# Kernel tuning notes

Measured on AMD Instinct MI355X. Metric: run time of the kernel, lower is better.

## Reference

```python
import jax, jax.numpy as jnp
import numpy as np

D = 1024
H = 16
HD = D // H
FF = 4096
EPS = 1e-5
B, L = 8, 1024

def setup_inputs() -> dict:
    key = jax.random.key(0)
    ks = jax.random.split(key, 12)
    s = lambda k, shape: jax.random.normal(k, shape, dtype=jnp.float32) * (shape[0] ** -0.5)
    return {
        "x": jax.random.normal(ks[0], (B, L, D), dtype=jnp.float32),
        "attention_mask": jnp.ones((B, L), dtype=jnp.int32),
        "wq": s(ks[1], (D, D)), "bq": jnp.zeros((D,), jnp.float32),
        "wk": s(ks[2], (D, D)), "bk": jnp.zeros((D,), jnp.float32),
        "wv": s(ks[3], (D, D)), "bv": jnp.zeros((D,), jnp.float32),
        "wo": s(ks[4], (D, D)), "bo": jnp.zeros((D,), jnp.float32),
        "ln1_s": jnp.ones((D,), jnp.float32), "ln1_b": jnp.zeros((D,), jnp.float32),
        "ln2_s": jnp.ones((D,), jnp.float32), "ln2_b": jnp.zeros((D,), jnp.float32),
        "w1": s(ks[5], (D, FF)), "b1": jnp.zeros((FF,), jnp.float32),
        "w2": s(ks[6], (FF, D)), "b2": jnp.zeros((D,), jnp.float32),
    }

def _layer_norm(x, scale, bias):
    mu = jnp.mean(x, axis=-1, keepdims=True)
    var = jnp.mean(jnp.square(x - mu), axis=-1, keepdims=True)
    return (x - mu) * jax.lax.rsqrt(var + EPS) * scale + bias

def _quick_gelu(x):
    return x * jax.nn.sigmoid(1.702 * x)

def reference(x, attention_mask, wq, bq, wk, bk, wv, bv, wo, bo,
              ln1_s, ln1_b, ln2_s, ln2_b, w1, b1, w2, b2):
    Bc, Lc, Dc = x.shape
    scale = HD ** -0.5
    # --- attention block (pre-LN) ---
    h = _layer_norm(x, ln1_s, ln1_b)
    to_heads = lambda t: t.reshape(Bc, Lc, H, HD).transpose(0, 2, 1, 3)
    q = to_heads(h @ wq + bq)
    k = to_heads(h @ wk + bk)
    v = to_heads(h @ wv + bv)
    scores = jnp.einsum('bhqd,bhkd->bhqk', q.astype(jnp.float32), k.astype(jnp.float32)) * scale
    fmask = jnp.where(attention_mask[:, None, None, :] > 0, 0.0,
                      jnp.finfo(scores.dtype).min)
    weights = jax.nn.softmax(scores + fmask, axis=-1)
    attn = jnp.einsum('bhqk,bhkd->bhqd', weights, v.astype(jnp.float32))
    attn = attn.transpose(0, 2, 1, 3).reshape(Bc, Lc, Dc).astype(x.dtype)
    x = x + (attn @ wo + bo)
    # --- MLP block (pre-LN) ---
    h = _layer_norm(x, ln2_s, ln2_b)
    h = _quick_gelu(h @ w1 + b1) @ w2 + b2
    return x + h
```

## Files before the change

kernel.cpp:

```cpp
#include <hip/hip_runtime.h>
#include <math.h>

#define D_MODEL 1024
#define N_TOK   8192
#define SEQ_L   1024
#define N_HEAD  16
#define HEAD_D  64
#define FF_DIM  4096

typedef __attribute__((ext_vector_type(8))) short bf16x8;
typedef __attribute__((ext_vector_type(4))) short short4v;
typedef __attribute__((ext_vector_type(2))) int  int2v;
typedef __attribute__((ext_vector_type(4))) float f32x4;

#define MFMA16(a, b, c) __builtin_amdgcn_mfma_f32_16x16x32_bf16((a), (b), (c), 0, 0, 0)

#define GLD16(gp, lp) __builtin_amdgcn_global_load_lds(                      \
    (const __attribute__((address_space(1))) void*)(gp),                     \
    (__attribute__((address_space(3))) void*)(lp), 16, 0, 0)

#if defined(__has_builtin)
#if __has_builtin(__builtin_amdgcn_exp2f)
#define EXP2F(x) __builtin_amdgcn_exp2f(x)
#else
#define EXP2F(x) exp2f(x)
#endif
#else
#define EXP2F(x) exp2f(x)
#endif

__device__ __forceinline__ short f2bf(float f) {
    unsigned u = __float_as_uint(f);
    u += 0x7fffu + ((u >> 16) & 1u);
    return (short)(u >> 16);
}

__device__ __forceinline__ int pack2bf(float a, float b) {
    unsigned ua = __float_as_uint(a) + 0x8000u;
    unsigned ub = __float_as_uint(b) + 0x8000u;
    return __builtin_amdgcn_perm(ub, ua, 0x07060302u);
}

__global__ __launch_bounds__(256) void ln_kernel(const float* __restrict__ x,
                                                 const float* __restrict__ g,
                                                 const float* __restrict__ b,
                                                 short* __restrict__ o)
{
    int t = blockIdx.x;
    const float* xr = x + (size_t)t * D_MODEL;
    short* orow = o + (size_t)t * D_MODEL;
    float vals[4];
    float lsum = 0.f, lsq = 0.f;
#pragma unroll
    for (int i = 0; i < 4; i++) {
        float v = xr[threadIdx.x + i * 256];
        vals[i] = v; lsum += v; lsq += v * v;
    }
#pragma unroll
    for (int off = 32; off > 0; off >>= 1) {
        lsum += __shfl_down(lsum, off);
        lsq  += __shfl_down(lsq,  off);
    }
    __shared__ float red[8];
    int wid = threadIdx.x >> 6, lane = threadIdx.x & 63;
    if (lane == 0) { red[wid] = lsum; red[4 + wid] = lsq; }
    __syncthreads();
    if (threadIdx.x == 0) {
        red[0] = red[0] + red[1] + red[2] + red[3];
        red[4] = red[4] + red[5] + red[6] + red[7];
    }
    __syncthreads();
    float mean = red[0] * (1.f / D_MODEL);
    float var  = red[4] * (1.f / D_MODEL) - mean * mean;
    float inv  = rsqrtf(var + 1e-5f);
#pragma unroll
    for (int i = 0; i < 4; i++) {
        int c = threadIdx.x + i * 256;
        orow[c] = f2bf((vals[i] - mean) * inv * g[c] + b[c]);
    }
}

__global__ __launch_bounds__(256) void prep_kernel(
    const float* __restrict__ wq, const float* __restrict__ wk,
    const float* __restrict__ wv, const float* __restrict__ wo,
    const float* __restrict__ w1, const float* __restrict__ w2,
    const int*   __restrict__ amask,
    short* __restrict__ wqkvt, short* __restrict__ wot,
    short* __restrict__ w1t,  short* __restrict__ w2t,
    float* __restrict__ fmask)
{
    int id = blockIdx.x;
    if (id >= 12288) {
        int i = (id - 12288) * 256 + threadIdx.x;
        fmask[i] = (amask[i] > 0) ? 0.f : -1e30f;
        return;
    }
    const float* src; short* dst; int R, C, tloc, csh;
    if (id < 4096) {
        int wsel = id >> 10; tloc = id & 1023; R = 1024; C = 1024; csh = 5;
        src = (wsel == 0) ? wq : (wsel == 1) ? wk : (wsel == 2) ? wv : wo;
        dst = (wsel == 3) ? wot : (wqkvt + (size_t)wsel * 1024 * 1024);
    } else if (id < 8192) {
        tloc = id - 4096; R = 1024; C = 4096; csh = 7; src = w1; dst = w1t;
    } else {
        tloc = id - 8192; R = 4096; C = 1024; csh = 5; src = w2; dst = w2t;
    }
    int ty = tloc >> csh, tx = tloc & ((1 << csh) - 1);
    int r0 = ty * 32, c0 = tx * 32;
    __shared__ float t[32][33];
    int tid = threadIdx.x;
#pragma unroll
    for (int i = 0; i < 4; i++) {
        int idx = i * 256 + tid;
        int r = idx >> 5, c = idx & 31;
        t[r][c] = src[(size_t)(r0 + r) * C + c0 + c];
    }
    __syncthreads();
#pragma unroll
    for (int i = 0; i < 4; i++) {
        int idx = i * 256 + tid;
        int rr = idx >> 5, cc = idx & 31;
        dst[(size_t)(c0 + rr) * R + r0 + cc] = f2bf(t[cc][rr]);
    }
}

template<int DBUF>
__global__ __launch_bounds__(256) void gemm_bf16(
    const short* __restrict__ A, int lda,
    const short* __restrict__ Bt, int ldb,
    const float* __restrict__ bias,
    const float* __restrict__ bias2,
    const float* __restrict__ bias3,
    const float* __restrict__ resid,
    float* __restrict__ Cf, short* __restrict__ Cb, short* __restrict__ Cvt,
    int ldc, int K, int act, int qkv, int gx)
{
    __shared__ __align__(16) short sA[(1 + DBUF) * 8192];
    __shared__ __align__(16) short sB[(1 + DBUF) * 8192];
    const int tid = threadIdx.x;
    const int lane = tid & 63, wave = tid >> 6;
    const int quad = lane >> 4, l15 = lane & 15;

    const int id = blockIdx.x;
    const int xcd = id & 7, j = id >> 3;
    const int bx = j % gx, by = xcd + 8 * (j / gx);
    const int bm = by * 128, bn = bx * 128;
    const int wm = (wave >> 1) * 64, wn = (wave & 1) * 64;

    const int lr = lane >> 3;
    const int lc = (lane & 7) ^ lr;
    const int sw = l15 & 7;

    const short* Ab = A  + (size_t)(bm + wave * 32 + lr) * lda + lc * 8;
    const short* Bb = Bt + (size_t)(bn + wave * 32 + lr) * ldb + lc * 8;

    f32x4 acc[4][4];
#pragma unroll
    for (int i = 0; i < 4; i++)
#pragma unroll
        for (int jj = 0; jj < 4; jj++) acc[i][jj] = (f32x4){0.f, 0.f, 0.f, 0.f};

    const int nk = K >> 6;

    if (DBUF) {
#pragma unroll
        for (int c = 0; c < 4; c++) {
            int cid = wave * 4 + c;
            GLD16(Ab + (size_t)(c * 8) * lda, &sA[cid * 512]);
            GLD16(Bb + (size_t)(c * 8) * ldb, &sB[cid * 512]);
        }
    }

    for (int ki = 0; ki < nk; ki++) {
        __syncthreads();
        if (DBUF) {
            if (ki + 1 < nk) {
                int k0 = (ki + 1) << 6, nb = (ki + 1) & 1;
#pragma unroll
                for (int c = 0; c < 4; c++) {
                    int cid = wave * 4 + c;
                    GLD16(Ab + (size_t)(c * 8) * lda + k0, &sA[nb * 8192 + cid * 512]);
                    GLD16(Bb + (size_t)(c * 8) * ldb + k0, &sB[nb * 8192 + cid * 512]);
                }
            }
        } else {
            int k0 = ki << 6;
#pragma unroll
            for (int c = 0; c < 4; c++) {
                int cid = wave * 4 + c;
                GLD16(Ab + (size_t)(c * 8) * lda + k0, &sA[cid * 512]);
                GLD16(Bb + (size_t)(c * 8) * ldb + k0, &sB[cid * 512]);
            }
            __syncthreads();
        }
        const short* cA = &sA[DBUF ? (ki & 1) * 8192 : 0];
        const short* cB = &sB[DBUF ? (ki & 1) * 8192 : 0];
#pragma unroll
        for (int ko = 0; ko < 2; ko++) {
            bf16x8 af[4], bfr[4];
#pragma unroll
            for (int mt = 0; mt < 4; mt++) {
                int row = wm + mt * 16 + l15;
                af[mt] = *(const bf16x8*)&cA[(row * 8 + ((ko * 4 + quad) ^ sw)) * 8];
            }
#pragma unroll
            for (int nt = 0; nt < 4; nt++) {
                int row = wn + nt * 16 + l15;
                bfr[nt] = *(const bf16x8*)&cB[(row * 8 + ((ko * 4 + quad) ^ sw)) * 8];
            }
#pragma unroll
            for (int mt = 0; mt < 4; mt++)
#pragma unroll
                for (int nt = 0; nt < 4; nt++)
                    acc[mt][nt] = MFMA16(af[mt], bfr[nt], acc[mt][nt]);
        }
    }

#pragma unroll
    for (int mt = 0; mt < 4; mt++)
#pragma unroll
        for (int nt = 0; nt < 4; nt++) {
            int row0 = bm + wm + mt * 16 + quad * 4;
            int col  = bn + wn + nt * 16 + l15;
            if (qkv) {
                int seg = col >> 10, cloc = col & 1023;
                const float* bp = (seg == 0) ? bias : (seg == 1) ? bias2 : bias3;
                float bval = bp[cloc];
                if (seg == 2) {
                    int bb = row0 >> 10, l0 = row0 & 1023;
                    size_t page = (size_t)(bb * N_HEAD + (cloc >> 6)) * HEAD_D + (cloc & 63);
                    short4v pk = { f2bf(acc[mt][nt][0] + bval), f2bf(acc[mt][nt][1] + bval),
                                   f2bf(acc[mt][nt][2] + bval), f2bf(acc[mt][nt][3] + bval) };
                    *(short4v*)&Cvt[page * SEQ_L + l0] = pk;
                } else {
                    short* dst = Cb + (size_t)seg * ((size_t)N_TOK * D_MODEL);
#pragma unroll
                    for (int r = 0; r < 4; r++)
                        dst[(size_t)(row0 + r) * D_MODEL + cloc] = f2bf(acc[mt][nt][r] + bval);
                }
            } else {
#pragma unroll
                for (int r = 0; r < 4; r++) {
                    int row = row0 + r;
                    float v = acc[mt][nt][r] + bias[col];
                    if (act) v = v / (1.f + __expf(-1.702f * v));
                    if (resid) v += resid[(size_t)row * ldc + col];
                    if (Cb) Cb[(size_t)row * ldc + col] = f2bf(v);
                    else    Cf[(size_t)row * ldc + col] = v;
                }
            }
        }
}

__global__ __launch_bounds__(256) void attn_kernel(
    const short* __restrict__ Q, const short* __restrict__ Kb,
    const short* __restrict__ Vt, const float* __restrict__ fmask,
    short* __restrict__ O)
{
    __shared__ __align__(16) short sK[8192];
    __shared__ __align__(16) short sV[8192];
    __shared__ __align__(16) short sP[4][32 * 136];
    __shared__ __align__(16) float sAl[4][2][20];

    const int g = blockIdx.x;
    const int xcd = g & 7, slot = g >> 3;
    const int qt = slot & 7, bhl = slot >> 3;
    const int bh = xcd * 16 + bhl;
    const int b = bh >> 4, h = bh & 15;

    const int tid = threadIdx.x;
    const int wave = tid >> 6, lane = tid & 63;
    const int quad = lane >> 4, l15 = lane & 15;

    const int qbase = b * SEQ_L + qt * 128;
    bf16x8 qf[2][2];
#pragma unroll
    for (int qh = 0; qh < 2; qh++) {
        const short* qp = Q + (size_t)(qbase + wave * 32 + qh * 16 + l15) * D_MODEL
                        + h * HEAD_D + quad * 8;
        qf[qh][0] = *(const bf16x8*)qp;
        qf[qh][1] = *(const bf16x8*)(qp + 32);
    }

    const short* Kbh = Kb + (size_t)b * SEQ_L * D_MODEL + h * HEAD_D;
    const short* Vbh = Vt + (size_t)(b * N_HEAD + h) * HEAD_D * SEQ_L;
    const float* mk  = fmask + b * SEQ_L;

    f32x4 o4[2][4];
#pragma unroll
    for (int qh = 0; qh < 2; qh++)
#pragma unroll
        for (int nt = 0; nt < 4; nt++) o4[qh][nt] = (f32x4){0.f, 0.f, 0.f, 0.f};
    float mrow[2] = {-1e30f, -1e30f}, lrow[2] = {0.f, 0.f};
    short* pslab = &sP[wave][0];
    const float CSC = 0.125f * 1.4426950408889634f;

    for (int kt = 0; kt < SEQ_L / 128; kt++) {
        __syncthreads();
#pragma unroll
        for (int j = 0; j < 4; j++) {
            int cid = wave * 4 + j;
            int kc = cid >> 1, key0 = (cid & 1) << 6;
            GLD16(Kbh + (size_t)(kt * 128 + key0 + lane) * D_MODEL + kc * 8,
                  &sK[cid * 512]);
            GLD16(Vbh + (size_t)lane * SEQ_L + kt * 128 + cid * 8,
                  &sV[cid * 512]);
        }
        __syncthreads();

        f32x4 mkv[8];
#pragma unroll
        for (int sub = 0; sub < 8; sub++)
            mkv[sub] = *(const f32x4*)&mk[kt * 128 + sub * 16 + quad * 4];

        f32x4 s[8][2];
#pragma unroll
        for (int sub = 0; sub < 8; sub++) {
            bf16x8 kf0 = *(const bf16x8*)&sK[(quad * 128 + sub * 16 + l15) * 8];
            bf16x8 kf1 = *(const bf16x8*)&sK[((quad + 4) * 128 + sub * 16 + l15) * 8];
#pragma unroll
            for (int qh = 0; qh < 2; qh++) {
                s[sub][qh] = (f32x4){0.f, 0.f, 0.f, 0.f};
                s[sub][qh] = MFMA16(kf0, qf[qh][0], s[sub][qh]);
                s[sub][qh] = MFMA16(kf1, qf[qh][1], s[sub][qh]);
            }
        }
        float alpha[2];
#pragma unroll
        for (int qh = 0; qh < 2; qh++) {
#pragma unroll
            for (int sub = 0; sub < 8; sub++)
#pragma unroll
                for (int r = 0; r < 4; r++)
                    s[sub][qh][r] = s[sub][qh][r] * CSC + mkv[sub][r];
            f32x4 mx4 = s[0][qh];
#pragma unroll
            for (int sub = 1; sub < 8; sub++)
#pragma unroll
                for (int r = 0; r < 4; r++) mx4[r] = fmaxf(mx4[r], s[sub][qh][r]);
            float pmax = fmaxf(fmaxf(mx4[0], mx4[1]), fmaxf(mx4[2], mx4[3]));
            pmax = fmaxf(pmax, __shfl_xor(pmax, 16));
            pmax = fmaxf(pmax, __shfl_xor(pmax, 32));
            float mnew = fmaxf(mrow[qh], pmax);
            alpha[qh] = EXP2F(mrow[qh] - mnew);
            mrow[qh] = mnew;
            if (quad == 0) sAl[wave][qh][l15] = alpha[qh];

            float ls = 0.f;
#pragma unroll
            for (int sub = 0; sub < 8; sub++) {
                float p0 = EXP2F(s[sub][qh][0] - mnew);
                float p1 = EXP2F(s[sub][qh][1] - mnew);
                float p2 = EXP2F(s[sub][qh][2] - mnew);
                float p3 = EXP2F(s[sub][qh][3] - mnew);
                ls += (p0 + p1) + (p2 + p3);
                int2v pk = { pack2bf(p0, p1), pack2bf(p2, p3) };
                *(int2v*)&pslab[(qh * 16 + l15) * 136 + sub * 16 + quad * 4] = pk;
            }
            ls += __shfl_xor(ls, 16);
            ls += __shfl_xor(ls, 32);
            lrow[qh] = lrow[qh] * alpha[qh] + ls;
        }

#pragma unroll
        for (int qh = 0; qh < 2; qh++) {
            f32x4 av = *(const f32x4*)&sAl[wave][qh][quad * 4];
#pragma unroll
            for (int nt = 0; nt < 4; nt++)
#pragma unroll
                for (int r = 0; r < 4; r++) o4[qh][nt][r] *= av[r];
        }

        bf16x8 pf[2][4];
#pragma unroll
        for (int qh = 0; qh < 2; qh++)
#pragma unroll
            for (int c = 0; c < 4; c++)
                pf[qh][c] = *(const bf16x8*)&pslab[(qh * 16 + l15) * 136 + c * 32 + quad * 8];
#pragma unroll
        for (int nt = 0; nt < 4; nt++)
#pragma unroll
            for (int c = 0; c < 4; c++) {
                bf16x8 vfr = *(const bf16x8*)&sV[((c * 4 + quad) * 64 + nt * 16 + l15) * 8];
                o4[0][nt] = MFMA16(pf[0][c], vfr, o4[0][nt]);
                o4[1][nt] = MFMA16(pf[1][c], vfr, o4[1][nt]);
            }
    }
    if (quad == 0) {
        sAl[wave][0][l15] = 1.f / lrow[0];
        sAl[wave][1][l15] = 1.f / lrow[1];
    }
    __syncthreads();
#pragma unroll
    for (int qh = 0; qh < 2; qh++) {
        f32x4 iv = *(const f32x4*)&sAl[wave][qh][quad * 4];
#pragma unroll
        for (int nt = 0; nt < 4; nt++)
#pragma unroll
            for (int r = 0; r < 4; r++)
                O[(size_t)(qbase + wave * 32 + qh * 16 + quad * 4 + r) * D_MODEL
                  + h * HEAD_D + nt * 16 + l15] = f2bf(o4[qh][nt][r] * iv[r]);
    }
}

extern "C" void kernel_launch(void* const* d_in, const int* in_sizes, int n_in,
                              void* d_out, int out_size, void* d_ws, size_t ws_size,
                              hipStream_t stream)
{
    const float* x     = (const float*)d_in[0];
    const int*   amask = (const int*)  d_in[1];
    const float* wq    = (const float*)d_in[2];
    const float* bq    = (const float*)d_in[3];
    const float* wk    = (const float*)d_in[4];
    const float* bk    = (const float*)d_in[5];
    const float* wv    = (const float*)d_in[6];
    const float* bv    = (const float*)d_in[7];
    const float* wo    = (const float*)d_in[8];
    const float* bo    = (const float*)d_in[9];
    const float* ln1s  = (const float*)d_in[10];
    const float* ln1b  = (const float*)d_in[11];
    const float* ln2s  = (const float*)d_in[12];
    const float* ln2b  = (const float*)d_in[13];
    const float* w1    = (const float*)d_in[14];
    const float* b1    = (const float*)d_in[15];
    const float* w2    = (const float*)d_in[16];
    const float* b2    = (const float*)d_in[17];
    float* out = (float*)d_out;

    char* w = (char*)d_ws;
    short* wqkvt = (short*)(w + (size_t)0);
    short* wot   = (short*)(w + ((size_t)6  << 20));
    short* w1t   = (short*)(w + ((size_t)8  << 20));
    short* w2t   = (short*)(w + ((size_t)16 << 20));
    short* hb    = (short*)(w + ((size_t)24 << 20));
    short* qb    = (short*)(w + ((size_t)40 << 20));
    short* kbf   = (short*)(w + ((size_t)56 << 20));
    short* attnb = (short*)(w + ((size_t)72 << 20));
    short* vtb   = (short*)(w + ((size_t)88 << 20));
    short* ffb   = qb;
    float* fmaskb = (float*)d_out;

    dim3 blk(256);

    prep_kernel<<<dim3(12320), blk, 0, stream>>>(wq, wk, wv, wo, w1, w2, amask,
                                                 wqkvt, wot, w1t, w2t, fmaskb);

    ln_kernel<<<N_TOK, blk, 0, stream>>>(x, ln1s, ln1b, hb);

    gemm_bf16<0><<<dim3(24 * 64), blk, 0, stream>>>(
        hb, 1024, wqkvt, 1024, bq, bk, bv, nullptr,
        nullptr, qb, vtb, 1024, 1024, 0, 1, 24);

    attn_kernel<<<dim3(1024), blk, 0, stream>>>(qb, kbf, vtb, fmaskb, attnb);

    gemm_bf16<1><<<dim3(8 * 64), blk, 0, stream>>>(
        attnb, 1024, wot, 1024, bo, nullptr, nullptr, x,
        out, nullptr, nullptr, 1024, 1024, 0, 0, 8);

    ln_kernel<<<N_TOK, blk, 0, stream>>>(out, ln2s, ln2b, hb);

    gemm_bf16<0><<<dim3(32 * 64), blk, 0, stream>>>(
        hb, 1024, w1t, 1024, b1, nullptr, nullptr, nullptr,
        nullptr, ffb, nullptr, 4096, 1024, 1, 0, 32);
    gemm_bf16<1><<<dim3(8 * 64), blk, 0, stream>>>(
        ffb, 4096, w2t, 4096, b2, nullptr, nullptr, out,
        out, nullptr, nullptr, 1024, 4096, 0, 0, 8);
}
```

Baseline: 537.5 us.

## Add 256-row, 512-thread bf16 GEMM with phased double-buffered pipeline

Adds a new gemm256 kernel with 256xBN tiles, 8 waves, and a hand-scheduled ping-pong schedule. It interleaves LDS fragment reads, MFMA phases (with raised priority), and global-to-LDS async loads under explicit barriers and waitcnts. The QKV, FFN-up and FFN-down GEMMs now use it in place of the 128-tile gemm_bf16. Larger tiles raise arithmetic intensity and the overlap hides load latency, at the cost of fewer blocks, heavier register and LDS use, and many barriers. The epilogue copied into the old kernel contains an odd duplicated Cf store that looks like an editing slip.

Result: slower. 748.2 us (+39.2%).

```diff
diff --git a/kernel.cpp b/kernel.cpp
--- a/kernel.cpp
+++ b/kernel.cpp
@@ -220,6 +220,193 @@
     for (int mt = 0; mt < 4; mt++)
 #pragma unroll
         for (int nt = 0; nt < 4; nt++) {
+            int row0 = bm + wm + mt * 16 + quad * 4;
+            int col  = bn + wn + nt * 16 + l15;
+            if (qkv) {
+                int seg = col >> 10, cloc = col & 1023;
+                const float* bp = (seg == 0) ? bias : (seg == 1) ? bias2 : bias3;
+                float bval = bp[cloc];
+                if (seg == 2) {
+                    int bb = row0 >> 10, l0 = row0 & 1023;
+                    size_t page = (size_t)(bb * N_HEAD + (cloc >> 6)) * HEAD_D + (cloc & 63);
+                    short4v pk = { f2bf(acc[mt][nt][0] + bval), f2bf(acc[mt][nt][1] + bval),
+                                   f2bf(acc[mt][nt][2] + bval), f2bf(acc[mt][nt][3] + bval) };
+                    *(short4v*)&Cvt[page * SEQ_L + l0] = pk;
+                } else {
+                    short* dst = Cb + (size_t)seg * ((size_t)N_TOK * D_MODEL);
+#pragma unroll
+                    for (int r = 0; r < 4; r++)
+                        dst[(size_t)(row0 + r) * D_MODEL + cloc] = f2bf(acc[mt][nt][r] + bval);
+                }
+            } else {
+#pragma unroll
+                for (int r = 0; r < 4; r++) {
+                    int row = row0 + r;
+                    float v = acc[mt][nt][r] + bias[col];
+                    if (act) v = v / (1.f + __expf(-1.702f * v));
+                    if (resid) v += resid[(size_t)row * ldc + col];
+                    if (Cb) Cb[(size_t)row * ldc + col] = f2bf(v);
+                    else    Cf[(size_t)row * ldc + col] = f2bf(v), Cf[(size_t)row * ldc + col] = v;
+                }
+            }
+        }
+}
+
+#define BAR() __builtin_amdgcn_s_barrier()
+#define WAIT_LGKM0() do { asm volatile("s_waitcnt lgkmcnt(0)");               \
+                          __builtin_amdgcn_sched_barrier(0); } while (0)
+
+#define STA(buf, h, tt) do {                                                  \
+    const short* s_ = Asrc + (size_t)((h) * 128) * lda + (size_t)(tt) * 64;   \
+    GLD16(s_,                    &sAs[(buf)*16384 + (h)*8192        + wave*512]); \
+    GLD16(s_ + (size_t)64 * lda, &sAs[(buf)*16384 + (h)*8192 + 4096 + wave*512]); \
+} while (0)
+
+#define STB(buf, h, tt) do {                                                  \
+    if constexpr (NREP == 4) {                                                \
+        const short* s_ = Bsrc + (size_t)((h) * 128) * ldb + (size_t)(tt) * 64; \
+        GLD16(s_,                    &sBs[(buf)*16384 + (h)*8192        + wave*512]); \
+        GLD16(s_ + (size_t)64 * ldb, &sBs[(buf)*16384 + (h)*8192 + 4096 + wave*512]); \
+    } else {                                                                  \
+        const short* s_ = Bsrc + (size_t)((h) * 64) * ldb + (size_t)(tt) * 64; \
+        GLD16(s_, &sBs[(buf)*8192 + (h)*4096 + wave*512]);                    \
+    }                                                                         \
+} while (0)
+
+#define VMCNT() do {                                                          \
+    if constexpr (NREP == 4) asm volatile("s_waitcnt vmcnt(6)");              \
+    else                     asm volatile("s_waitcnt vmcnt(4)");              \
+} while (0)
+
+#define LDA_F(buf, mt, ko) (*(const bf16x8*)&sAs[(buf)*16384 +                \
+    (((wm + (mt)*16 + l15) << 3) + (((ko)*4 + quad) ^ sw)) * 8])
+#define LDB_F(buf, nt, ko) (*(const bf16x8*)&sBs[(buf)*(NREP == 4 ? 16384 : 8192) + \
+    (((wn + (nt)*16 + l15) << 3) + (((ko)*4 + quad) ^ sw)) * 8])
+
+#define PH_READ_B(buf)                                                        \
+    _Pragma("unroll")                                                         \
+    for (int nt = 0; nt < NREP; nt++) {                                       \
+        bfr[nt][0] = LDB_F(buf, nt, 0);                                       \
+        bfr[nt][1] = LDB_F(buf, nt, 1);                                       \
+    }
+#define PH_READ_A(buf, mh)                                                    \
+    _Pragma("unroll")                                                         \
+    for (int mt = 0; mt < 4; mt++) {                                          \
+        afr[mt][0] = LDA_F(buf, (mh)*4 + mt, 0);                              \
+        afr[mt][1] = LDA_F(buf, (mh)*4 + mt, 1);                              \
+    }
+#define PH_MFMA(mh, nh)                                                       \
+    __builtin_amdgcn_s_setprio(1);                                            \
+    _Pragma("unroll")                                                         \
+    for (int mt = 0; mt < 4; mt++)                                            \
+        _Pragma("unroll")                                                     \
+        for (int nt = 0; nt < NREP / 2; nt++) {                               \
+            acc[(mh)*4 + mt][(nh)*(NREP/2) + nt] =                            \
+                MFMA16(afr[mt][0], bfr[(nh)*(NREP/2) + nt][0],                \
+                       acc[(mh)*4 + mt][(nh)*(NREP/2) + nt]);                 \
+            acc[(mh)*4 + mt][(nh)*(NREP/2) + nt] =                            \
+                MFMA16(afr[mt][1], bfr[(nh)*(NREP/2) + nt][1],                \
+                       acc[(mh)*4 + mt][(nh)*(NREP/2) + nt]);                 \
+        }                                                                     \
+    __builtin_amdgcn_s_setprio(0);
+
+template<int NREP>
+__global__ __launch_bounds__(512, 2) void gemm256(
+    const short* __restrict__ A, int lda,
+    const short* __restrict__ Bt, int ldb,
+    const float* __restrict__ bias,
+    const float* __restrict__ bias2,
+    const float* __restrict__ bias3,
+    const float* __restrict__ resid,
+    float* __restrict__ Cf, short* __restrict__ Cb, short* __restrict__ Cvt,
+    int ldc, int K, int act, int qkv, int gx)
+{
+    constexpr int BN = NREP * 64;
+    __shared__ __align__(16) short sAs[2 * 256 * 64];
+    __shared__ __align__(16) short sBs[2 * BN  * 64];
+
+    const int tid  = threadIdx.x;
+    const int wave = tid >> 6, lane = tid & 63;
+    const int quad = lane >> 4, l15 = lane & 15;
+    const int wm = (wave >> 2) * 128;
+    const int wn = (wave & 3) * (NREP * 16);
+    const int sw = l15 & 7;
+
+    const int id = blockIdx.x;
+    const int xcd = id & 7, j = id >> 3;
+    const int bx = j % gx, by = xcd + 8 * (j / gx);
+    const int bm = by * 256, bn = bx * BN;
+
+    const int r_in = tid >> 3;
+    const int csrc = (tid & 7) ^ (r_in & 7);
+    const short* Asrc = A  + (size_t)(bm + r_in) * lda + csrc * 8;
+    const short* Bsrc = Bt + (size_t)(bn + r_in) * ldb + csrc * 8;
+
+    f32x4 acc[8][NREP];
+#pragma unroll
+    for (int i = 0; i < 8; i++)
+#pragma unroll
+        for (int jj = 0; jj < NREP; jj++) acc[i][jj] = (f32x4){0.f, 0.f, 0.f, 0.f};
+
+    const int nk = K >> 6;
+
+    STB(0, 0, 0); STB(0, 1, 0);
+    STA(0, 0, 0); STA(0, 1, 0);
+    STB(1, 0, 1); STB(1, 1, 1);
+    STA(1, 0, 1);
+    VMCNT();
+    BAR();
+
+    bf16x8 afr[4][2], bfr[NREP][2];
+
+    for (int it = 0; it < nk; it += 2) {
+        int t2 = it + 2; if (t2 >= nk) t2 -= nk;
+        int t3 = it + 3; if (t3 >= nk) t3 -= nk;
+
+        PH_READ_B(0); PH_READ_A(0, 0);
+        STA(1, 1, it + 1);
+        BAR(); WAIT_LGKM0();
+        PH_MFMA(0, 0);
+        BAR();
+        STB(0, 0, t2);
+        BAR();
+        PH_MFMA(0, 1);
+        BAR();
+        PH_READ_A(0, 1);
+        STB(0, 1, t2);
+        BAR(); WAIT_LGKM0();
+        PH_MFMA(1, 1);
+        BAR();
+        STA(0, 0, t2);
+        BAR();
+        PH_MFMA(1, 0);
+        VMCNT();
+        BAR();
+        PH_READ_B(1); PH_READ_A(1, 0);
+        STA(0, 1, t2);
+        BAR(); WAIT_LGKM0();
+        PH_MFMA(0, 0);
+        BAR();
+        STB(1, 0, t3);
+        BAR();
+        PH_MFMA(0, 1);
+        BAR();
+        PH_READ_A(1, 1);
+        STB(1, 1, t3);
+        BAR(); WAIT_LGKM0();
+        PH_MFMA(1, 1);
+        BAR();
+        STA(1, 0, t3);
+        BAR();
+        PH_MFMA(1, 0);
+        VMCNT();
+        BAR();
+    }
+
+#pragma unroll
+    for (int mt = 0; mt < 8; mt++)
+#pragma unroll
+        for (int nt = 0; nt < NREP; nt++) {
             int row0 = bm + wm + mt * 16 + quad * 4;
             int col  = bn + wn + nt * 16 + l15;
             if (qkv) {
@@ -440,16 +627,16 @@
     short* ffb   = qb;
     float* fmaskb = (float*)d_out;
 
-    dim3 blk(256);
+    dim3 blk(256), blk512(512);
 
     prep_kernel<<<dim3(12320), blk, 0, stream>>>(wq, wk, wv, wo, w1, w2, amask,
                                                  wqkvt, wot, w1t, w2t, fmaskb);
 
     ln_kernel<<<N_TOK, blk, 0, stream>>>(x, ln1s, ln1b, hb);
 
-    gemm_bf16<0><<<dim3(24 * 64), blk, 0, stream>>>(
+    gemm256<4><<<dim3(384), blk512, 0, stream>>>(
         hb, 1024, wqkvt, 1024, bq, bk, bv, nullptr,
-        nullptr, qb, vtb, 1024, 1024, 0, 1, 24);
+        nullptr, qb, vtb, 1024, 1024, 0, 1, 12);
 
     attn_kernel<<<dim3(1024), blk, 0, stream>>>(qb, kbf, vtb, fmaskb, attnb);
 
@@ -459,10 +646,10 @@
 
     ln_kernel<<<N_TOK, blk, 0, stream>>>(out, ln2s, ln2b, hb);
 
-    gemm_bf16<0><<<dim3(32 * 64), blk, 0, stream>>>(
+    gemm256<4><<<dim3(512), blk512, 0, stream>>>(
         hb, 1024, w1t, 1024, b1, nullptr, nullptr, nullptr,
-        nullptr, ffb, nullptr, 4096, 1024, 1, 0, 32);
-    gemm_bf16<1><<<dim3(8 * 64), blk, 0, stream>>>(
+        nullptr, ffb, nullptr, 4096, 1024, 1, 0, 16);
+    gemm256<2><<<dim3(256), blk512, 0, stream>>>(
         ffb, 4096, w2t, 4096, b2, nullptr, nullptr, out,
         out, nullptr, nullptr, 1024, 4096, 0, 0, 8);
 }
```
